# Kernel tuning notes

Measured on AMD Instinct MI355X. Metric: run time of the kernel, lower is better.

The kernel has to match this reference:

```python
import jax, jax.numpy as jnp
import numpy as np

NUM_USER = 1000
NUM_NODES = 3000
NUM_REL = 5
HID = 500
OUT = 75
NUM_BASIS = 2
NUM_EDGES = 200000


def setup_inputs() -> dict:
    key = jax.random.key(0)
    ks = jax.random.split(key, 8)
    x = jnp.arange(NUM_NODES, dtype=jnp.int64 if jax.config.jax_enable_x64 else jnp.int32)
    edge_index = jax.random.randint(ks[0], (2, NUM_EDGES), 0, NUM_NODES)
    edge_type = jax.random.randint(ks[1], (NUM_EDGES,), 0, NUM_REL)
    edge_norm = jax.random.uniform(ks[2], (NUM_EDGES,), dtype=jnp.float32)
    # RGC ordinal basis weights: W_r = cumsum of per-relation bases (GCMC ordinal weight sharing)
    ord_basis = 0.01 * jax.random.normal(ks[3], (NUM_REL, NUM_NODES, HID), dtype=jnp.float32)
    # DenseLayer weight (no bias), shared for user/item branches
    W_dense = 0.05 * jax.random.normal(ks[4], (HID, OUT), dtype=jnp.float32)
    # BiDecoder basis decomposition
    basis_matrix = 0.1 * jax.random.normal(ks[5], (NUM_BASIS, OUT * OUT), dtype=jnp.float32)
    coefs = 0.1 * jax.random.normal(ks[6], (NUM_REL, NUM_BASIS), dtype=jnp.float32)
    return {"x": x, "edge_index": edge_index, "edge_type": edge_type,
            "edge_norm": edge_norm, "ord_basis": ord_basis, "W_dense": W_dense,
            "basis_matrix": basis_matrix, "coefs": coefs}


def reference(x, edge_index, edge_type, edge_norm, ord_basis, W_dense, basis_matrix, coefs):
    R, N, H = ord_basis.shape
    # --- RGCLayer: ordinal cumulative weight sharing ---
    weight = jnp.cumsum(ord_basis, axis=0).reshape(R * N, H)  # (R*N, H)
    src, dst = edge_index[0], edge_index[1]
    idx = edge_type * N + x[src]                      # row lookup = one-hot feature matmul
    msgs = weight[idx] * edge_norm[:, None]           # (E, H) gather, memory-bound
    agg = jax.ops.segment_sum(msgs, dst, num_segments=N)  # scatter-add to target nodes
    feat = jax.nn.relu(agg)                           # (N, H)
    # --- separate users / items, DenseLayer ---
    u = jax.nn.relu(feat[:NUM_USER] @ W_dense)        # (U, OUT)
    i = jax.nn.relu(feat[NUM_USER:] @ W_dense)        # (I, OUT)
    # --- BiDecoder: basis-combination bilinear scores per relation ---
    D = W_dense.shape[1]
    Q = jnp.einsum('rb,bk->rk', coefs, basis_matrix).reshape(R, D, D)
    out = jnp.einsum('ud,rde,ie->uir', u, Q, i)       # (U, I, R)
    return out.reshape(u.shape[0] * i.shape[0], R)
```

## Files before the change

### kernel.cpp

```cpp
#include <hip/hip_runtime.h>
#include <hip/hip_bf16.h>

#define NUSER 1000
#define NNODES 3000
#define NREL 5
#define HID 500
#define DOUT 75
#define NBASIS 2
#define NEDGES 200000
#define NITEM (NNODES - NUSER)
#define NH (NNODES * HID)
#define ROWF4 125

__global__ void k_cumsum(const float4* __restrict__ basis, float4* __restrict__ weight,
                         int* __restrict__ deg) {
    int i = blockIdx.x * blockDim.x + threadIdx.x;
    if (i < NNODES) deg[i] = 0;
    if (i >= NH / 4) return;
    float4 s = make_float4(0.f, 0.f, 0.f, 0.f);
#pragma unroll
    for (int r = 0; r < NREL; ++r) {
        float4 b = basis[r * (NH / 4) + i];
        s.x += b.x; s.y += b.y; s.z += b.z; s.w += b.w;
        weight[r * (NH / 4) + i] = s;
    }
}

__global__ void k_degree(const int* __restrict__ dst, int* __restrict__ deg) {
    int e = blockIdx.x * blockDim.x + threadIdx.x;
    if (e < NEDGES) atomicAdd(&deg[dst[e]], 1);
}

__global__ __launch_bounds__(1024) void k_scan(const int* __restrict__ deg,
                                               int* __restrict__ offs,
                                               int* __restrict__ cursor) {
    __shared__ int wsum[16];
    int t = threadIdx.x;
    int base = t * 3;
    int a = (base     < NNODES) ? deg[base]     : 0;
    int b = (base + 1 < NNODES) ? deg[base + 1] : 0;
    int c = (base + 2 < NNODES) ? deg[base + 2] : 0;
    int s = a + b + c;
    int lane = t & 63, wid = t >> 6;
    int v = s;
#pragma unroll
    for (int d = 1; d < 64; d <<= 1) {
        int x = __shfl_up(v, d);
        if (lane >= d) v += x;
    }
    if (lane == 63) wsum[wid] = v;
    __syncthreads();
    if (t < 16) {
        int w = wsum[t];
#pragma unroll
        for (int d = 1; d < 16; d <<= 1) {
            int x = __shfl_up(w, d);
            if (t >= d) w += x;
        }
        wsum[t] = w;
    }
    __syncthreads();
    int woff = wid ? wsum[wid - 1] : 0;
    int incl = v + woff;
    int excl = incl - s;
    if (base < NNODES)     { offs[base]     = excl;         cursor[base]     = excl; }
    if (base + 1 < NNODES) { offs[base + 1] = excl + a;     cursor[base + 1] = excl + a; }
    if (base + 2 < NNODES) { offs[base + 2] = excl + a + b; cursor[base + 2] = excl + a + b; }
    if (t == 1023) offs[NNODES] = incl;
}

__global__ void k_fill(const int* __restrict__ src, const int* __restrict__ dst,
                       const int* __restrict__ etype, const float* __restrict__ enorm,
                       const int* __restrict__ x,
                       int* __restrict__ cursor, int* __restrict__ csr_row,
                       float* __restrict__ csr_norm) {
    int e = blockIdx.x * blockDim.x + threadIdx.x;
    if (e >= NEDGES) return;
    int d = dst[e];
    int pos = atomicAdd(&cursor[d], 1);
    csr_row[pos] = etype[e] * NNODES + x[src[e]];
    csr_norm[pos] = enorm[e];
}

__global__ __launch_bounds__(256) void k_agg(const float4* __restrict__ w4,
                                             const int* __restrict__ offs,
                                             const int* __restrict__ csr_row,
                                             const float* __restrict__ csr_norm,
                                             float4* __restrict__ feat4) {
    __shared__ float4 part[16][16];
    int bid = blockIdx.x;
    int s = bid & 7;
    int n = bid >> 3;
    int t = threadIdx.x;
    int g = t >> 4;
    int lane = t & 15;
    int wdt = (s < 7) ? 16 : 13;
    int boff = s * 16;
    int beg = offs[n], end = offs[n + 1];
    float4 acc = make_float4(0.f, 0.f, 0.f, 0.f);
    if (lane < wdt) {
        for (int p = beg + g; p < end; p += 16) {
            int row = csr_row[p];
            float wn = csr_norm[p];
            float4 v = w4[(size_t)row * ROWF4 + boff + lane];
            acc.x += v.x * wn; acc.y += v.y * wn; acc.z += v.z * wn; acc.w += v.w * wn;
        }
    }
    part[g][lane] = acc;
    __syncthreads();
#pragma unroll
    for (int st = 8; st >= 1; st >>= 1) {
        if (g < st) {
            float4 o = part[g + st][lane];
            float4 m = part[g][lane];
            m.x += o.x; m.y += o.y; m.z += o.z; m.w += o.w;
            part[g][lane] = m;
        }
        __syncthreads();
    }
    if (g == 0 && lane < wdt) {
        float4 m = part[0][lane];
        m.x = fmaxf(m.x, 0.f); m.y = fmaxf(m.y, 0.f);
        m.z = fmaxf(m.z, 0.f); m.w = fmaxf(m.w, 0.f);
        feat4[(size_t)n * ROWF4 + boff + lane] = m;
    }
}

#define DN 8
__global__ __launch_bounds__(256) void k_dense(const float* __restrict__ feat,
                                               const float* __restrict__ W,
                                               float* __restrict__ uv) {
    __shared__ float lds[DN][HID];
    int nb = blockIdx.x * DN;
    int t = threadIdx.x;
    const float4* f4 = (const float4*)(feat + (size_t)nb * HID);
    float4* l4 = (float4*)&lds[0][0];
    for (int j = t; j < DN * HID / 4; j += 256) l4[j] = f4[j];
    __syncthreads();
    if (t < 225) {
        int g = t / 75, o = t % 75;
        float a0 = 0.f, a1 = 0.f, a2 = 0.f;
        for (int d = 0; d < HID; ++d) {
            float w = W[d * DOUT + o];
            a0 += lds[g][d] * w;
            a1 += lds[g + 3][d] * w;
            a2 += lds[(g + 6) & 7][d] * w;
        }
        uv[(nb + g) * DOUT + o]     = fmaxf(a0, 0.f);
        uv[(nb + g + 3) * DOUT + o] = fmaxf(a1, 0.f);
        if (g < 2) uv[(nb + g + 6) * DOUT + o] = fmaxf(a2, 0.f);
    }
}

__global__ void k_T(const float* __restrict__ uv, const float* __restrict__ bm,
                    float* __restrict__ T) {
    int i = blockIdx.x * blockDim.x + threadIdx.x;
    if (i >= NBASIS * NUSER * DOUT) return;
    int b = i / (NUSER * DOUT);
    int rem = i % (NUSER * DOUT);
    int u = rem / DOUT;
    int e = rem % DOUT;
    float acc = 0.f;
    for (int d = 0; d < DOUT; ++d)
        acc += uv[u * DOUT + d] * bm[b * DOUT * DOUT + d * DOUT + e];
    T[i] = acc;
}

#define UT 32
#define IT 128
#define EC 25
__global__ __launch_bounds__(256) void k_dec(const float* __restrict__ T,
                                             const float* __restrict__ uv,
                                             const float* __restrict__ coefs,
                                             float* __restrict__ out) {
    __shared__ float As[NBASIS][UT][EC];
    __shared__ float Is[IT][EC];
    int t = threadIdx.x;
    int ti = t & 31;
    int tu = t >> 5;
    int ub = blockIdx.y * UT;
    int ib = blockIdx.x * IT;

    float acc[NBASIS][4][4] = {};

    for (int e0 = 0; e0 < DOUT; e0 += EC) {
        for (int j = t; j < NBASIS * UT * EC; j += 256) {
            int b = j / (UT * EC);
            int rem = j % (UT * EC);
            int uu = rem / EC, c = rem % EC;
            int u = ub + uu;
            As[b][uu][c] = (u < NUSER) ? T[(b * NUSER + u) * DOUT + e0 + c] : 0.f;
        }
        for (int j = t; j < IT * EC; j += 256) {
            int ii = j / EC, c = j % EC;
            int i = ib + ii;
            Is[ii][c] = (i < NITEM) ? uv[(size_t)(NUSER + i) * DOUT + e0 + c] : 0.f;
        }
        __syncthreads();
        for (int c = 0; c < EC; ++c) {
            float av[NBASIS][4];
#pragma unroll
            for (int b = 0; b < NBASIS; ++b)
#pragma unroll
                for (int uu = 0; uu < 4; ++uu)
                    av[b][uu] = As[b][tu * 4 + uu][c];
            float iv[4];
#pragma unroll
            for (int k = 0; k < 4; ++k) iv[k] = Is[ti + 32 * k][c];
#pragma unroll
            for (int b = 0; b < NBASIS; ++b)
#pragma unroll
                for (int uu = 0; uu < 4; ++uu)
#pragma unroll
                    for (int k = 0; k < 4; ++k)
                        acc[b][uu][k] += av[b][uu] * iv[k];
        }
        __syncthreads();
    }

    float cf[NREL][NBASIS];
#pragma unroll
    for (int r = 0; r < NREL; ++r)
#pragma unroll
        for (int b = 0; b < NBASIS; ++b) cf[r][b] = coefs[r * NBASIS + b];

#pragma unroll
    for (int uu = 0; uu < 4; ++uu) {
        int u = ub + tu * 4 + uu;
        if (u >= NUSER) continue;
#pragma unroll
        for (int k = 0; k < 4; ++k) {
            int i = ib + ti + 32 * k;
            if (i >= NITEM) continue;
            size_t base = ((size_t)u * NITEM + i) * NREL;
            float s0 = acc[0][uu][k], s1 = acc[1][uu][k];
#pragma unroll
            for (int r = 0; r < NREL; ++r)
                out[base + r] = cf[r][0] * s0 + cf[r][1] * s1;
        }
    }
}

extern "C" void kernel_launch(void* const* d_in, const int* in_sizes, int n_in,
                              void* d_out, int out_size, void* d_ws, size_t ws_size,
                              hipStream_t stream) {
    const int*   x     = (const int*)d_in[0];
    const int*   ei    = (const int*)d_in[1];
    const int*   etype = (const int*)d_in[2];
    const float* enorm = (const float*)d_in[3];
    const float* basis = (const float*)d_in[4];
    const float* Wd    = (const float*)d_in[5];
    const float* bm    = (const float*)d_in[6];
    const float* coefs = (const float*)d_in[7];
    float* out = (float*)d_out;

    float* weight   = (float*)d_ws;
    float* feat     = weight + 7500000;
    float* uv       = feat + 1500000;
    float* T        = uv + 225000;
    float* csr_norm = T + 150000;
    int*   csr_row  = (int*)(csr_norm + 200000);
    int*   deg      = csr_row + 200000;
    int*   offs     = deg + 3000;
    int*   cursor   = offs + 3001;

    const int* src = ei;
    const int* dst = ei + NEDGES;

    k_cumsum<<<(NH / 4 + 255) / 256, 256, 0, stream>>>((const float4*)basis,
                                                       (float4*)weight, deg);
    k_degree<<<(NEDGES + 255) / 256, 256, 0, stream>>>(dst, deg);
    k_scan<<<1, 1024, 0, stream>>>(deg, offs, cursor);
    k_fill<<<(NEDGES + 255) / 256, 256, 0, stream>>>(src, dst, etype, enorm, x, cursor,
                                                     csr_row, csr_norm);
    k_agg<<<NNODES * 8, 256, 0, stream>>>((const float4*)weight, offs, csr_row, csr_norm,
                                          (float4*)feat);
    k_dense<<<NNODES / DN, 256, 0, stream>>>(feat, Wd, uv);
    k_T<<<(NBASIS * NUSER * DOUT + 255) / 256, 256, 0, stream>>>(uv, bm, T);
    k_dec<<<dim3((NITEM + IT - 1) / IT, (NUSER + UT - 1) / UT), 256, 0, stream>>>(T, uv, coefs, out);
}
```

Before: 262.7 us.

## Assign one node per 16-thread group in aggregation, drop LDS reduction

The aggregation kernel now gives each node a single 16-lane group, which walks all of that node's edges serially. Each block covers 16 nodes for one column slice instead of one node. This removes the shared-memory tree reduction and its repeated __syncthreads, and cuts the block count by 16x. In exchange each group runs a long serial loop of about 67 edges with fewer loads in flight. Degree imbalance across nodes in the same block may also leave lanes idle.

```diff
diff --git a/kernel.cpp b/kernel.cpp
--- a/kernel.cpp
+++ b/kernel.cpp
@@ -87,42 +87,33 @@
                                              const int* __restrict__ csr_row,
                                              const float* __restrict__ csr_norm,
                                              float4* __restrict__ feat4) {
-    __shared__ float4 part[16][16];
     int bid = blockIdx.x;
     int s = bid & 7;
-    int n = bid >> 3;
+    int chunk = bid >> 3;
     int t = threadIdx.x;
     int g = t >> 4;
     int lane = t & 15;
+    int n = chunk * 16 + g;
+    if (n >= NNODES) return;
     int wdt = (s < 7) ? 16 : 13;
     int boff = s * 16;
     int beg = offs[n], end = offs[n + 1];
+    bool act = lane < wdt;
     float4 acc = make_float4(0.f, 0.f, 0.f, 0.f);
-    if (lane < wdt) {
-        for (int p = beg + g; p < end; p += 16) {
-            int row = csr_row[p];
-            float wn = csr_norm[p];
+#pragma unroll 4
+    for (int p = beg; p < end; ++p) {
+        int row = csr_row[p];
+        float wn = csr_norm[p];
+        if (act) {
             float4 v = w4[(size_t)row * ROWF4 + boff + lane];
-            acc.x += v.x * wn; acc.y += v.y * wn; acc.z += v.z * wn; acc.w += v.w * wn;
-        }
-    }
-    part[g][lane] = acc;
-    __syncthreads();
-#pragma unroll
-    for (int st = 8; st >= 1; st >>= 1) {
-        if (g < st) {
-            float4 o = part[g + st][lane];
-            float4 m = part[g][lane];
-            m.x += o.x; m.y += o.y; m.z += o.z; m.w += o.w;
-            part[g][lane] = m;
-        }
-        __syncthreads();
-    }
-    if (g == 0 && lane < wdt) {
-        float4 m = part[0][lane];
-        m.x = fmaxf(m.x, 0.f); m.y = fmaxf(m.y, 0.f);
-        m.z = fmaxf(m.z, 0.f); m.w = fmaxf(m.w, 0.f);
-        feat4[(size_t)n * ROWF4 + boff + lane] = m;
+            acc.x += v.x * wn; acc.y += v.y * wn;
+            acc.z += v.z * wn; acc.w += v.w * wn;
+        }
+    }
+    if (act) {
+        acc.x = fmaxf(acc.x, 0.f); acc.y = fmaxf(acc.y, 0.f);
+        acc.z = fmaxf(acc.z, 0.f); acc.w = fmaxf(acc.w, 0.f);
+        feat4[(size_t)n * ROWF4 + boff + lane] = acc;
     }
 }
 
@@ -273,8 +264,8 @@
     k_scan<<<1, 1024, 0, stream>>>(deg, offs, cursor);
     k_fill<<<(NEDGES + 255) / 256, 256, 0, stream>>>(src, dst, etype, enorm, x, cursor,
                                                      csr_row, csr_norm);
-    k_agg<<<NNODES * 8, 256, 0, stream>>>((const float4*)weight, offs, csr_row, csr_norm,
-                                          (float4*)feat);
+    k_agg<<<((NNODES + 15) / 16) * 8, 256, 0, stream>>>((const float4*)weight, offs,
+                                                        csr_row, csr_norm, (float4*)feat);
     k_dense<<<NNODES / DN, 256, 0, stream>>>(feat, Wd, uv);
     k_T<<<(NBASIS * NUSER * DOUT + 255) / 256, 256, 0, stream>>>(uv, bm, T);
     k_dec<<<dim3((NITEM + IT - 1) / IT, (NUSER + UT - 1) / UT), 256, 0, stream>>>(T, uv, coefs, out);
```

New measurement: 272.1 us. +3.6%, slower.
